# Performance work log

Hardware: AMD Instinct MI355X
Metric: run time of the kernel (lower is better)

## Reference

```python
import jax, jax.numpy as jnp
import numpy as np
from jax import lax

DN = ('NCHW', 'OIHW', 'NCHW')

def conv(x, w, b, stride):
    y = lax.conv_general_dilated(x, w, (stride, stride), ((1, 1), (1, 1)), dimension_numbers=DN)
    return y + b[None, :, None, None]

def deconv(x, w, b):
    # PyTorch ConvTranspose2d(k=3, stride=2, padding=1, output_padding=1): doubles H, W.
    # w has torch layout [in, out, kH, kW]; convert to OIHW and flip spatially.
    wt = jnp.flip(w, (-2, -1)).transpose(1, 0, 2, 3)
    y = lax.conv_general_dilated(x, wt, (1, 1), ((1, 2), (1, 2)), lhs_dilation=(2, 2), dimension_numbers=DN)
    return y + b[None, :, None, None]


def setup_inputs() -> dict:
    key = jax.random.key(0)
    ks = jax.random.split(key, 16)
    s = 0.05
    d = {
        'x': jax.random.normal(ks[0], (16, 3, 256, 256), jnp.float32),
        'w1': jax.random.normal(ks[1], (64, 3, 3, 3), jnp.float32) * s,
        'b1': jnp.zeros((64,), jnp.float32),
        'w2': jax.random.normal(ks[2], (128, 64, 3, 3), jnp.float32) * s,
        'b2': jnp.zeros((128,), jnp.float32),
        'w3': jax.random.normal(ks[3], (256, 128, 3, 3), jnp.float32) * s,
        'b3': jnp.zeros((256,), jnp.float32),
        'w4': jax.random.normal(ks[4], (512, 256, 3, 3), jnp.float32) * s,
        'b4': jnp.zeros((512,), jnp.float32),
        'codebook': jax.random.normal(ks[5], (8192, 512), jnp.float32),
        # ConvTranspose2d weights in torch layout [in, out, kH, kW]
        'd1w': jax.random.normal(ks[6], (512, 256, 3, 3), jnp.float32) * s,
        'd1b': jnp.zeros((256,), jnp.float32),
        'd2w': jax.random.normal(ks[7], (256, 128, 3, 3), jnp.float32) * s,
        'd2b': jnp.zeros((128,), jnp.float32),
        'd3w': jax.random.normal(ks[8], (128, 64, 3, 3), jnp.float32) * s,
        'd3b': jnp.zeros((64,), jnp.float32),
        'wo': jax.random.normal(ks[9], (3, 64, 3, 3), jnp.float32) * s,
        'bo': jnp.zeros((3,), jnp.float32),
    }
    return d


def reference(x, w1, b1, w2, b2, w3, b3, w4, b4, codebook, d1w, d1b, d2w, d2b, d3w, d3b, wo, bo):
    # Encoder: 256 -> 256 -> 128 -> 64 -> 32 spatial
    h = jax.nn.relu(conv(x, w1, b1, 1))
    h = jax.nn.relu(conv(h, w2, b2, 2))
    h = jax.nn.relu(conv(h, w3, b3, 2))
    z = conv(h, w4, b4, 2)  # [B, 512, 32, 32]

    # Quantize: nearest codebook entry per spatial vector (channels-last).
    B, C, H, W = z.shape
    zf = z.transpose(0, 2, 3, 1).reshape(-1, C)  # [N, 512]
    # squared euclidean distances; argmin identical to cdist argmin
    d2 = (jnp.sum(zf * zf, axis=-1, keepdims=True)
          - 2.0 * (zf @ codebook.T)
          + jnp.sum(codebook * codebook, axis=-1))  # [N, K]
    indices = jnp.argmin(d2, axis=-1)  # [N]
    zq = codebook[indices].reshape(B, H, W, C).transpose(0, 3, 1, 2)  # [B, 512, 32, 32]

    # Decoder: 32 -> 64 -> 128 -> 256
    g = jax.nn.relu(deconv(zq, d1w, d1b))
    g = jax.nn.relu(deconv(g, d2w, d2b))
    g = jax.nn.relu(deconv(g, d3w, d3b))
    x_recon = jax.nn.sigmoid(conv(g, wo, bo, 1))
    return x_recon, indices
```

## Files before the change

kernel.cpp:

```cpp
#include <hip/hip_runtime.h>
#include <cstddef>

typedef short short8 __attribute__((ext_vector_type(8)));
typedef _Float16 half8 __attribute__((ext_vector_type(8)));
typedef _Float16 half4 __attribute__((ext_vector_type(4)));
typedef _Float16 half2v __attribute__((ext_vector_type(2)));
typedef float floatx4 __attribute__((ext_vector_type(4)));

__device__ __forceinline__ unsigned short f2bf(float f) {
    unsigned u = __float_as_uint(f);
    u += 0x7FFFu + ((u >> 16) & 1u);
    return (unsigned short)(u >> 16);
}
__device__ __forceinline__ float bf2f(unsigned short h) {
    return __uint_as_float((unsigned)h << 16);
}

__global__ __launch_bounds__(256)
void fused_conv12_mfma_kernel(const float* __restrict__ x,
                              const float* __restrict__ w1,
                              const float* __restrict__ b1,
                              const _Float16* __restrict__ w2h,
                              const _Float16* __restrict__ w2l,
                              const float* __restrict__ b2,
                              _Float16* __restrict__ outH,
                              _Float16* __restrict__ outL)
{
    __shared__ float s_x[3][11][36];
    __shared__ _Float16 sE[2][9][17][40];
    __shared__ _Float16 sO[2][9][16][40];

    const int tid = threadIdx.x;
    const int lane = tid & 63;
    const int wave = tid >> 6;
    const int n16 = lane & 15;
    const int quad = lane >> 4;

    const int ox0 = (blockIdx.x & 7) * 16;
    const int oy0 = (blockIdx.x >> 3) * 4;
    const int co0 = blockIdx.y * 64 + wave * 16;
    const int img = blockIdx.z;

    const int hy0 = oy0 * 2 - 1, hx0 = ox0 * 2 - 1;
    const int gy0 = hy0 - 1,     gx0 = hx0 - 1;
    const float* xN = x + (size_t)img * 3 * 65536;

    for (int e = tid; e < 3 * 11 * 35; e += 256) {
        int c = e / 385, r = e % 385;
        int yy = r / 35, xx = r % 35;
        int gy = gy0 + yy, gx = gx0 + xx;
        float v = 0.f;
        if ((unsigned)gy < 256u && (unsigned)gx < 256u)
            v = xN[(size_t)c * 65536 + gy * 256 + gx];
        s_x[c][yy][xx] = v;
    }

    floatx4 acc1[4], acc2[4];
#pragma unroll
    for (int s = 0; s < 4; s++) {
        acc1[s] = (floatx4){0.f, 0.f, 0.f, 0.f};
        acc2[s] = (floatx4){0.f, 0.f, 0.f, 0.f};
    }

    const int pair = tid & 15;
    const int pxg  = tid >> 4;

    for (int c0 = 0; c0 < 64; c0 += 32) {
        __syncthreads();

        const int ch0 = c0 + pair * 2;
        float wA[27], wB[27];
#pragma unroll
        for (int k = 0; k < 27; k++) {
            wA[k] = w1[ch0 * 27 + k];
            wB[k] = w1[ch0 * 27 + 27 + k];
        }
        const float bA = b1[ch0], bB = b1[ch0 + 1];

        for (int px = pxg; px < 33; px += 16) {
            const bool colok = (unsigned)(hx0 + px) < 256u;
            float xw[3][3][3];
#pragma unroll
            for (int c = 0; c < 3; c++)
#pragma unroll
                for (int r = 0; r < 3; r++)
#pragma unroll
                    for (int kx = 0; kx < 3; kx++)
                        xw[c][r][kx] = s_x[c][r][px + kx];
#pragma unroll
            for (int py = 0; py < 9; py++) {
                const bool inb = colok && (unsigned)(hy0 + py) < 256u;
                float aA = bA, aB = bB;
#pragma unroll
                for (int c = 0; c < 3; c++)
#pragma unroll
                    for (int k = 0; k < 9; k++) {
                        const float xv = xw[c][k / 3][k % 3];
                        aA += wA[c * 9 + k] * xv;
                        aB += wB[c * 9 + k] * xv;
                    }
                float vA = inb ? fmaxf(aA, 0.f) : 0.f;
                float vB = inb ? fmaxf(aB, 0.f) : 0.f;
                half2v hv, lv;
                _Float16 hA = (_Float16)vA, hB = (_Float16)vB;
                hv[0] = hA; hv[1] = hB;
                lv[0] = (_Float16)((vA - (float)hA) * 1024.f);
                lv[1] = (_Float16)((vB - (float)hB) * 1024.f);
                _Float16* dH = (px & 1) ? &sO[0][py][px >> 1][pair * 2]
                                        : &sE[0][py][px >> 1][pair * 2];
                _Float16* dL = (px & 1) ? &sO[1][py][px >> 1][pair * 2]
                                        : &sE[1][py][px >> 1][pair * 2];
                *(half2v*)dH = hv;
                *(half2v*)dL = lv;
                if (py < 8) {
#pragma unroll
                    for (int c = 0; c < 3; c++) {
#pragma unroll
                        for (int r = 0; r < 2; r++)
#pragma unroll
                            for (int kx = 0; kx < 3; kx++)
                                xw[c][r][kx] = xw[c][r + 1][kx];
#pragma unroll
                        for (int kx = 0; kx < 3; kx++)
                            xw[c][2][kx] = s_x[c][py + 3][px + kx];
                    }
                }
            }
        }
        __syncthreads();

        half8 ah[9], al[9];
#pragma unroll
        for (int tp = 0; tp < 9; tp++) {
            size_t o = ((size_t)(tp * 128 + co0 + n16)) * 64 + c0 + quad * 8;
            ah[tp] = *(const half8*)(w2h + o);
            al[tp] = *(const half8*)(w2l + o);
        }
#pragma unroll
        for (int oy = 0; oy < 4; oy++) {
#pragma unroll
            for (int tp = 0; tp < 9; tp++) {
                const int kx = tp % 3;
                const int row = oy * 2 + tp / 3;
                half8 bh, bl;
                if (kx == 0)      { bh = *(const half8*)&sE[0][row][n16][quad * 8];
                                    bl = *(const half8*)&sE[1][row][n16][quad * 8]; }
                else if (kx == 1) { bh = *(const half8*)&sO[0][row][n16][quad * 8];
                                    bl = *(const half8*)&sO[1][row][n16][quad * 8]; }
                else              { bh = *(const half8*)&sE[0][row][n16 + 1][quad * 8];
                                    bl = *(const half8*)&sE[1][row][n16 + 1][quad * 8]; }
                acc1[oy] = __builtin_amdgcn_mfma_f32_16x16x32_f16(ah[tp], bh, acc1[oy], 0, 0, 0);
                acc2[oy] = __builtin_amdgcn_mfma_f32_16x16x32_f16(ah[tp], bl, acc2[oy], 0, 0, 0);
                acc2[oy] = __builtin_amdgcn_mfma_f32_16x16x32_f16(al[tp], bh, acc2[oy], 0, 0, 0);
            }
        }
    }

    const float4 bv = *(const float4*)&b2[co0 + quad * 4];
    const float bb[4] = {bv.x, bv.y, bv.z, bv.w};
#pragma unroll
    for (int oy = 0; oy < 4; oy++) {
        half4 hv, lv;
#pragma unroll
        for (int r = 0; r < 4; r++) {
            float v = fmaxf(acc1[oy][r] + acc2[oy][r] * (1.0f / 1024.0f) + bb[r], 0.f);
            _Float16 h = (_Float16)v;
            hv[r] = h;
            lv[r] = (_Float16)((v - (float)h) * 1024.f);
        }
        size_t o = (((size_t)img * 128 + (oy0 + oy)) * 128 + (ox0 + n16)) * 128
                   + co0 + quad * 4;
        *(half4*)(outH + o) = hv;
        *(half4*)(outL + o) = lv;
    }
}

template<int CI, int CO>
__global__ __launch_bounds__(256)
void prepack_conv_kernel(const float* __restrict__ w,
                         _Float16* __restrict__ wh, _Float16* __restrict__ wl)
{
    int i = blockIdx.x * 256 + threadIdx.x;
    if (i >= CO * CI * 9) return;
    int co = i / (CI * 9);
    int r  = i % (CI * 9);
    int ci = r / 9;
    int tp = r % 9;
    float v = w[i];
    _Float16 h = (_Float16)v;
    size_t o = ((size_t)tp * CO + co) * CI + ci;
    wh[o] = h;
    wl[o] = (_Float16)((v - (float)h) * 1024.f);
}

template<int CIN, int COUT, int IH, int IW, bool RELU>
__global__ __launch_bounds__(256)
void conv_mfma_kernel(const _Float16* __restrict__ inH, const _Float16* __restrict__ inL,
                      const _Float16* __restrict__ wpH, const _Float16* __restrict__ wpL,
                      const float* __restrict__ bias,
                      _Float16* __restrict__ outH, _Float16* __restrict__ outL)
{
    constexpr int OH = IH / 2, OW = IW / 2;
    __shared__ _Float16 sE[2][9][17][40];
    __shared__ _Float16 sO[2][9][16][40];

    const int tid = threadIdx.x;
    const int lane = tid & 63;
    const int wave = tid >> 6;
    const int n16 = lane & 15;
    const int quad = lane >> 4;

    constexpr int NTX = OW / 16;
    const int ox0 = (blockIdx.x % NTX) * 16;
    const int oy0 = (blockIdx.x / NTX) * 4;
    const int co0 = blockIdx.y * 64 + wave * 16;
    const int img = blockIdx.z;

    const int iy0 = oy0 * 2 - 1;
    const int ix0 = ox0 * 2 - 1;
    const _Float16* iNH = inH + (size_t)img * IH * IW * CIN;
    const _Float16* iNL = inL + (size_t)img * IH * IW * CIN;

    floatx4 acc1[4], acc2[4];
#pragma unroll
    for (int s = 0; s < 4; s++) {
        acc1[s] = (floatx4){0.f, 0.f, 0.f, 0.f};
        acc2[s] = (floatx4){0.f, 0.f, 0.f, 0.f};
    }

    for (int k0 = 0; k0 < CIN; k0 += 32) {
        __syncthreads();
        for (int e = tid; e < 2376; e += 256) {
            int pl = e / 1188;
            int r  = e % 1188;
            int pix = r >> 2, q = r & 3;
            int py = pix / 33, px = pix % 33;
            int iy = iy0 + py, ix = ix0 + px;
            half8 v = (half8)(_Float16)0;
            if ((unsigned)iy < (unsigned)IH && (unsigned)ix < (unsigned)IW)
                v = *(const half8*)((pl ? iNL : iNH) + ((size_t)(iy * IW + ix) * CIN + k0 + q * 8));
            if (px & 1) *(half8*)&sO[pl][py][px >> 1][q * 8] = v;
            else        *(half8*)&sE[pl][py][px >> 1][q * 8] = v;
        }
        __syncthreads();

        half8 ah[9], al[9];
#pragma unroll
        for (int tp = 0; tp < 9; tp++) {
            size_t o = ((size_t)(tp * COUT + co0 + n16)) * CIN + k0 + quad * 8;
            ah[tp] = *(const half8*)(wpH + o);
            al[tp] = *(const half8*)(wpL + o);
        }

#pragma unroll
        for (int oy = 0; oy < 4; oy++) {
#pragma unroll
            for (int tp = 0; tp < 9; tp++) {
                const int ky = tp / 3, kx = tp % 3;
                const int row = oy * 2 + ky;
                half8 bh, bl;
                if (kx == 0)      { bh = *(const half8*)&sE[0][row][n16][quad * 8];
                                    bl = *(const half8*)&sE[1][row][n16][quad * 8]; }
                else if (kx == 1) { bh = *(const half8*)&sO[0][row][n16][quad * 8];
                                    bl = *(const half8*)&sO[1][row][n16][quad * 8]; }
                else              { bh = *(const half8*)&sE[0][row][n16 + 1][quad * 8];
                                    bl = *(const half8*)&sE[1][row][n16 + 1][quad * 8]; }
                acc1[oy] = __builtin_amdgcn_mfma_f32_16x16x32_f16(ah[tp], bh, acc1[oy], 0, 0, 0);
                acc2[oy] = __builtin_amdgcn_mfma_f32_16x16x32_f16(ah[tp], bl, acc2[oy], 0, 0, 0);
                acc2[oy] = __builtin_amdgcn_mfma_f32_16x16x32_f16(al[tp], bh, acc2[oy], 0, 0, 0);
            }
        }
    }

    const float4 bv = *(const float4*)&bias[co0 + quad * 4];
    const float bb[4] = {bv.x, bv.y, bv.z, bv.w};
#pragma unroll
    for (int oy = 0; oy < 4; oy++) {
        half4 hv, lv;
#pragma unroll
        for (int r = 0; r < 4; r++) {
            float v = acc1[oy][r] + acc2[oy][r] * (1.0f / 1024.0f) + bb[r];
            if (RELU) v = fmaxf(v, 0.f);
            _Float16 h = (_Float16)v;
            hv[r] = h;
            lv[r] = (_Float16)((v - (float)h) * 1024.f);
        }
        size_t o = (((size_t)img * OH + (oy0 + oy)) * OW + (ox0 + n16)) * COUT
                   + co0 + quad * 4;
        *(half4*)(outH + o) = hv;
        *(half4*)(outL + o) = lv;
    }
}

__global__ __launch_bounds__(64)
void cnorm_kernel(const float* __restrict__ cb, float* __restrict__ cn)
{
    const int code = blockIdx.x;
    const int t = threadIdx.x;
    const float* row = cb + (size_t)code * 512;
    float s = 0.f;
    for (int i = t; i < 512; i += 64) s += row[i] * row[i];
#pragma unroll
    for (int off = 32; off > 0; off >>= 1) s += __shfl_down(s, off, 64);
    if (t == 0) cn[code] = s;
}

__global__ __launch_bounds__(256)
void init_keys_kernel(unsigned long long* __restrict__ keys)
{
    keys[blockIdx.x * 256 + threadIdx.x] = ~0ull;
}

__global__ __launch_bounds__(256)
void split_cb_kernel(const float* __restrict__ cb,
                     _Float16* __restrict__ ch, _Float16* __restrict__ cl)
{
    size_t i = (size_t)blockIdx.x * 256 + threadIdx.x;
    float v = cb[i];
    _Float16 h = (_Float16)v;
    ch[i] = h;
    cl[i] = (_Float16)((v - (float)h) * 1024.f);
}

__global__ __launch_bounds__(256)
void vq_mfma_kernel(const _Float16* __restrict__ zh, const _Float16* __restrict__ zl,
                    const _Float16* __restrict__ ch, const _Float16* __restrict__ cl,
                    const float* __restrict__ cn,
                    unsigned long long* __restrict__ keys)
{
    __shared__ _Float16 sB[2][512 * 8];

    const int tid = threadIdx.x;
    const int lane = tid & 63;
    const int wave = tid >> 6;
    const int n16 = lane & 15;
    const int quad = lane >> 4;

    const int code0 = blockIdx.x * 64;
    const int row0 = blockIdx.y * 256 + wave * 64;

    floatx4 acc1[4][4], acc2[4][4];
#pragma unroll
    for (int rt = 0; rt < 4; rt++)
#pragma unroll
        for (int ct = 0; ct < 4; ct++) {
            acc1[rt][ct] = (floatx4){0.f, 0.f, 0.f, 0.f};
            acc2[rt][ct] = (floatx4){0.f, 0.f, 0.f, 0.f};
        }

    const _Float16* pzh = zh + (size_t)(row0 + n16) * 512 + quad * 8;
    const _Float16* pzl = zl + (size_t)(row0 + n16) * 512 + quad * 8;

    const int e0 = tid, e1 = tid + 256;
    const _Float16* s0 = ((e0 >> 8) ? cl : ch)
        + (size_t)(code0 + ((e0 >> 6) & 3) * 16 + ((e0 >> 2) & 15)) * 512 + (e0 & 3) * 8;
    const _Float16* s1 = ((e1 >> 8) ? cl : ch)
        + (size_t)(code0 + ((e1 >> 6) & 3) * 16 + ((e1 >> 2) & 15)) * 512 + (e1 & 3) * 8;

    *(half8*)&sB[0][e0 * 8] = *(const half8*)s0;
    *(half8*)&sB[0][e1 * 8] = *(const half8*)s1;
    __syncthreads();

    for (int c = 0; c < 16; ++c) {
        const int cur = c & 1;
        const int kk = c * 32;
        half8 ah[4], al[4];
#pragma unroll
        for (int rt = 0; rt < 4; rt++) {
            ah[rt] = *(const half8*)(pzh + (size_t)rt * 8192 + kk);
            al[rt] = *(const half8*)(pzl + (size_t)rt * 8192 + kk);
        }
        half8 t0, t1;
        if (c < 15) {
            t0 = *(const half8*)(s0 + kk + 32);
            t1 = *(const half8*)(s1 + kk + 32);
        }
#pragma unroll
        for (int ct = 0; ct < 4; ++ct) {
            half8 bh = *(const half8*)&sB[cur][(ct * 64 + n16 * 4 + quad) * 8];
            half8 bl = *(const half8*)&sB[cur][(256 + ct * 64 + n16 * 4 + quad) * 8];
#pragma unroll
            for (int rt = 0; rt < 4; rt++) {
                acc1[rt][ct] = __builtin_amdgcn_mfma_f32_16x16x32_f16(ah[rt], bh, acc1[rt][ct], 0, 0, 0);
                acc2[rt][ct] = __builtin_amdgcn_mfma_f32_16x16x32_f16(ah[rt], bl, acc2[rt][ct], 0, 0, 0);
                acc2[rt][ct] = __builtin_amdgcn_mfma_f32_16x16x32_f16(al[rt], bh, acc2[rt][ct], 0, 0, 0);
            }
        }
        if (c < 15) {
            const int nxt = cur ^ 1;
            *(half8*)&sB[nxt][e0 * 8] = t0;
            *(half8*)&sB[nxt][e1 * 8] = t1;
        }
        __syncthreads();
    }

#pragma unroll
    for (int rt = 0; rt < 4; rt++) {
#pragma unroll
        for (int reg = 0; reg < 4; reg++) {
            float best = 3.0e38f;
            int bcode = 0;
#pragma unroll
            for (int ct = 0; ct < 4; ct++) {
                const int code = code0 + ct * 16 + n16;
                float dot = acc1[rt][ct][reg] + acc2[rt][ct][reg] * (1.0f / 1024.0f);
                float s = cn[code] - 2.0f * dot;
                if (s < best) { best = s; bcode = code; }
            }
            unsigned u = __float_as_uint(best);
            u = (u & 0x80000000u) ? ~u : (u | 0x80000000u);
            unsigned long long key = ((unsigned long long)u << 32) | (unsigned)bcode;
#pragma unroll
            for (int m = 1; m < 16; m <<= 1) {
                unsigned long long o = __shfl_xor(key, m, 64);
                key = (o < key) ? o : key;
            }
            if (n16 == 0)
                atomicMin(&keys[row0 + rt * 16 + quad * 4 + reg], key);
        }
    }
}

__global__ __launch_bounds__(256)
void vq_gather_kernel(const unsigned long long* __restrict__ keys,
                      const float* __restrict__ cb,
                      unsigned short* __restrict__ zq, float* __restrict__ idx_out)
{
    __shared__ int sidx[64];
    const int t = threadIdx.x;
    const int v0 = blockIdx.x * 64;
    if (t < 64) {
        int idx = (int)(keys[v0 + t] & 0xFFFFFFFFull);
        sidx[t] = idx;
        idx_out[v0 + t] = (float)idx;
    }
    __syncthreads();
    const int tv = t >> 2;
    const int q = t & 3;
    const float* crow = cb + (size_t)sidx[tv] * 512;
    unsigned short* zrow = zq + (size_t)(v0 + tv) * 512;
    for (int c = q * 8; c < 512; c += 32) {
        float4 f0 = *(const float4*)(crow + c);
        float4 f1 = *(const float4*)(crow + c + 4);
        short8 h;
        h[0] = (short)f2bf(f0.x); h[1] = (short)f2bf(f0.y);
        h[2] = (short)f2bf(f0.z); h[3] = (short)f2bf(f0.w);
        h[4] = (short)f2bf(f1.x); h[5] = (short)f2bf(f1.y);
        h[6] = (short)f2bf(f1.z); h[7] = (short)f2bf(f1.w);
        *(short8*)(zrow + c) = h;
    }
}

template<int CI, int CO>
__global__ __launch_bounds__(256)
void prepack_kernel(const float* __restrict__ w, unsigned short* __restrict__ wp)
{
    int i = blockIdx.x * 256 + threadIdx.x;
    if (i >= 9 * CO * CI) return;
    int ci = i / (CO * 9);
    int r  = i % (CO * 9);
    int co = r / 9;
    int tp = r % 9;
    wp[((size_t)tp * CO + co) * CI + ci] = f2bf(w[i]);
}

template<int CIN, int COUT, int IH, int IW, bool OUT_NCHW>
__global__ __launch_bounds__(256)
void deconv_mfma_kernel(const unsigned short* __restrict__ in,
                        const unsigned short* __restrict__ wp,
                        const float* __restrict__ bias,
                        unsigned short* __restrict__ out)
{
    constexpr int OH = 2 * IH, OW = 2 * IW;
    __shared__ short sIn[5][17][40];

    const int tid = threadIdx.x;
    const int lane = tid & 63;
    const int wave = tid >> 6;
    const int n16 = lane & 15;
    const int quad = lane >> 4;

    constexpr int NTX = IW / 16;
    const int x0 = (blockIdx.x % NTX) * 16;
    const int y0 = (blockIdx.x / NTX) * 4;
    const int co0 = blockIdx.y * 64 + wave * 16;
    const int img = blockIdx.z;

    const unsigned short* inN = in + (size_t)img * IH * IW * CIN;

    floatx4 acc[4][4];
#pragma unroll
    for (int s = 0; s < 4; s++)
#pragma unroll
        for (int c = 0; c < 4; c++) acc[s][c] = (floatx4){0.f, 0.f, 0.f, 0.f};

    for (int k0 = 0; k0 < CIN; k0 += 32) {
        __syncthreads();
        for (int e = tid; e < 340; e += 256) {
            int yy = e / 68, r = e % 68;
            int xx = r >> 2, q4 = r & 3;
            int gy = y0 + yy, gx = x0 + xx;
            short8 v = {0, 0, 0, 0, 0, 0, 0, 0};
            if (gy < IH && gx < IW)
                v = *(const short8*)(inN + ((size_t)(gy * IW + gx) * CIN + k0 + q4 * 8));
            *(short8*)&sIn[yy][xx][q4 * 8] = v;
        }
        __syncthreads();

        short8 a[9];
#pragma unroll
        for (int tp = 0; tp < 9; tp++)
            a[tp] = *(const short8*)(wp + ((size_t)(tp * COUT + co0 + n16) * CIN + k0 + quad * 8));

#pragma unroll
        for (int s = 0; s < 4; s++) {
            short8 b00 = *(const short8*)&sIn[s    ][n16    ][quad * 8];
            short8 b01 = *(const short8*)&sIn[s    ][n16 + 1][quad * 8];
            short8 b10 = *(const short8*)&sIn[s + 1][n16    ][quad * 8];
            short8 b11 = *(const short8*)&sIn[s + 1][n16 + 1][quad * 8];
            acc[s][0] = __builtin_amdgcn_mfma_f32_16x16x32_bf16(a[4], b00, acc[s][0], 0, 0, 0);
            acc[s][1] = __builtin_amdgcn_mfma_f32_16x16x32_bf16(a[3], b01, acc[s][1], 0, 0, 0);
            acc[s][1] = __builtin_amdgcn_mfma_f32_16x16x32_bf16(a[5], b00, acc[s][1], 0, 0, 0);
            acc[s][2] = __builtin_amdgcn_mfma_f32_16x16x32_bf16(a[1], b10, acc[s][2], 0, 0, 0);
            acc[s][2] = __builtin_amdgcn_mfma_f32_16x16x32_bf16(a[7], b00, acc[s][2], 0, 0, 0);
            acc[s][3] = __builtin_amdgcn_mfma_f32_16x16x32_bf16(a[0], b11, acc[s][3], 0, 0, 0);
            acc[s][3] = __builtin_amdgcn_mfma_f32_16x16x32_bf16(a[2], b10, acc[s][3], 0, 0, 0);
            acc[s][3] = __builtin_amdgcn_mfma_f32_16x16x32_bf16(a[6], b01, acc[s][3], 0, 0, 0);
            acc[s][3] = __builtin_amdgcn_mfma_f32_16x16x32_bf16(a[8], b00, acc[s][3], 0, 0, 0);
        }
    }

    const float4 bv = *(const float4*)&bias[co0 + quad * 4];
    const float bb[4] = {bv.x, bv.y, bv.z, bv.w};
    const int x = x0 + n16;

    if (!OUT_NCHW) {
        unsigned short* outN = out + (size_t)img * OH * OW * COUT;
#pragma unroll
        for (int s = 0; s < 4; s++) {
            const int y = y0 + s;
#pragma unroll
            for (int c = 0; c < 4; c++) {
                const int oy = 2 * y + (c >> 1);
                const int ox = 2 * x + (c & 1);
                ushort4 h;
                h.x = f2bf(fmaxf(acc[s][c][0] + bb[0], 0.f));
                h.y = f2bf(fmaxf(acc[s][c][1] + bb[1], 0.f));
                h.z = f2bf(fmaxf(acc[s][c][2] + bb[2], 0.f));
                h.w = f2bf(fmaxf(acc[s][c][3] + bb[3], 0.f));
                *(ushort4*)(outN + ((size_t)(oy * OW + ox) * COUT + co0 + quad * 4)) = h;
            }
        }
    } else {
#pragma unroll
        for (int s = 0; s < 4; s++) {
            const int y = y0 + s;
#pragma unroll
            for (int r = 0; r < 4; r++) {
                const int co = co0 + quad * 4 + r;
                unsigned short* oC = out + (size_t)(img * COUT + co) * OH * OW;
                unsigned p0 = (unsigned)f2bf(fmaxf(acc[s][0][r] + bb[r], 0.f)) |
                              ((unsigned)f2bf(fmaxf(acc[s][1][r] + bb[r], 0.f)) << 16);
                unsigned p1 = (unsigned)f2bf(fmaxf(acc[s][2][r] + bb[r], 0.f)) |
                              ((unsigned)f2bf(fmaxf(acc[s][3][r] + bb[r], 0.f)) << 16);
                *(unsigned*)(oC + (size_t)(2 * y) * OW + 2 * x) = p0;
                *(unsigned*)(oC + (size_t)(2 * y + 1) * OW + 2 * x) = p1;
            }
        }
    }
}

__global__ __launch_bounds__(256)
void conv_out_kernel(const unsigned short* __restrict__ in,
                     const float* __restrict__ w,
                     const float* __restrict__ bias,
                     float* __restrict__ out)
{
    constexpr int TIC = 4;
    __shared__ float s_in[TIC][3][258];
    const int t = threadIdx.x;
    const int y = blockIdx.x;
    const int n = blockIdx.y;
    const unsigned short* inN = in + (size_t)n * 64 * 65536;
    float acc0 = bias[0], acc1 = bias[1], acc2 = bias[2];

    for (int c0 = 0; c0 < 64; c0 += TIC) {
        for (int e = t; e < TIC * 3 * 258; e += 256) {
            int ci = e / 774;
            int r  = e % 774;
            int ry = r / 258, xx = r % 258;
            int gy = y - 1 + ry, gx = xx - 1;
            float v = 0.f;
            if ((unsigned)gy < 256u && (unsigned)gx < 256u)
                v = bf2f(inN[(size_t)(c0 + ci) * 65536 + gy * 256 + gx]);
            s_in[ci][ry][xx] = v;
        }
        __syncthreads();
#pragma unroll
        for (int ci = 0; ci < TIC; ++ci) {
            float iv[3][3];
#pragma unroll
            for (int ry = 0; ry < 3; ry++)
#pragma unroll
                for (int kx = 0; kx < 3; kx++)
                    iv[ry][kx] = s_in[ci][ry][t + kx];
#pragma unroll
            for (int k = 0; k < 9; k++) {
                const float v = iv[k / 3][k % 3];
                acc0 += w[(0 * 64 + c0 + ci) * 9 + k] * v;
                acc1 += w[(1 * 64 + c0 + ci) * 9 + k] * v;
                acc2 += w[(2 * 64 + c0 + ci) * 9 + k] * v;
            }
        }
        __syncthreads();
    }
    const size_t o = (size_t)((n * 3 + 0) * 256 + y) * 256 + t;
    out[o]          = 1.f / (1.f + __expf(-acc0));
    out[o + 65536]  = 1.f / (1.f + __expf(-acc1));
    out[o + 131072] = 1.f / (1.f + __expf(-acc2));
}

extern "C" void kernel_launch(void* const* d_in, const int* in_sizes, int n_in,
                              void* d_out, int out_size, void* d_ws, size_t ws_size,
                              hipStream_t stream)
{
    const float* x   = (const float*)d_in[0];
    const float* w1  = (const float*)d_in[1];
    const float* b1  = (const float*)d_in[2];
    const float* w2  = (const float*)d_in[3];
    const float* b2  = (const float*)d_in[4];
    const float* w3  = (const float*)d_in[5];
    const float* b3  = (const float*)d_in[6];
    const float* w4  = (const float*)d_in[7];
    const float* b4  = (const float*)d_in[8];
    const float* cb  = (const float*)d_in[9];
    const float* d1w = (const float*)d_in[10];
    const float* d1b = (const float*)d_in[11];
    const float* d2w = (const float*)d_in[12];
    const float* d2b = (const float*)d_in[13];
    const float* d3w = (const float*)d_in[14];
    const float* d3b = (const float*)d_in[15];
    const float* wo  = (const float*)d_in[16];
    const float* bo  = (const float*)d_in[17];

    char* ws = (char*)d_ws;
    _Float16* H2H = (_Float16*)(ws);
    _Float16* H2L = (_Float16*)(ws + 67108864);
    _Float16* H3H = (_Float16*)(ws + 134217728);
    _Float16* H3L = (_Float16*)(ws + 167772160);
    _Float16* ZH  = (_Float16*)(ws);
    _Float16* ZL  = (_Float16*)(ws + 16777216);
    unsigned short* ZQ = (unsigned short*)(ws + 33554432);
    _Float16* CBH = (_Float16*)(ws + 50331648);
    _Float16* CBL = (_Float16*)(ws + 58720256);
    unsigned short* G1 = (unsigned short*)(ws + 67108864);
    unsigned short* G2 = (unsigned short*)(ws + 134217728);
    unsigned short* G3 = (unsigned short*)(ws);
    unsigned long long* keys = (unsigned long long*)(ws + 201326592);
    float* cn = (float*)(ws + 201326592 + 131072);

    char* oscratch = (char*)d_out;
    _Float16* EW3H = (_Float16*)(oscratch);
    _Float16* EW3L = (_Float16*)(oscratch + 589824);
    _Float16* EW4H = (_Float16*)(oscratch + 1179648);
    _Float16* EW4L = (_Float16*)(oscratch + 3538944);
    unsigned short* WP1 = (unsigned short*)(oscratch + 5898240);
    unsigned short* WP2 = (unsigned short*)(oscratch + 8257536);
    unsigned short* WP3 = (unsigned short*)(oscratch + 8847360);
    _Float16* EW2H = (_Float16*)(oscratch + 8994816);
    _Float16* EW2L = (_Float16*)(oscratch + 9142272);

    float* xrec = (float*)d_out;
    float* idxf = (float*)d_out + (size_t)16 * 3 * 256 * 256;

    prepack_conv_kernel<64,  128><<<288,  256, 0, stream>>>(w2, EW2H, EW2L);
    prepack_conv_kernel<128, 256><<<1152, 256, 0, stream>>>(w3, EW3H, EW3L);
    prepack_conv_kernel<256, 512><<<4608, 256, 0, stream>>>(w4, EW4H, EW4L);
    prepack_kernel<512, 256><<<4608, 256, 0, stream>>>(d1w, WP1);
    prepack_kernel<256, 128><<<1152, 256, 0, stream>>>(d2w, WP2);
    prepack_kernel<128, 64 ><<<288,  256, 0, stream>>>(d3w, WP3);

    fused_conv12_mfma_kernel<<<dim3(256, 2, 16), 256, 0, stream>>>(x, w1, b1, EW2H, EW2L, b2, H2H, H2L);
    conv_mfma_kernel<128, 256, 128, 128, true ><<<dim3(64, 4, 16), 256, 0, stream>>>(H2H, H2L, EW3H, EW3L, b3, H3H, H3L);
    conv_mfma_kernel<256, 512, 64,  64,  false><<<dim3(16, 8, 16), 256, 0, stream>>>(H3H, H3L, EW4H, EW4L, b4, ZH, ZL);

    cnorm_kernel<<<8192, 64, 0, stream>>>(cb, cn);
    init_keys_kernel<<<64, 256, 0, stream>>>(keys);
    split_cb_kernel<<<16384, 256, 0, stream>>>(cb, CBH, CBL);
    vq_mfma_kernel<<<dim3(128, 64), 256, 0, stream>>>(ZH, ZL, CBH, CBL, cn, keys);
    vq_gather_kernel<<<256, 256, 0, stream>>>(keys, cb, ZQ, idxf);

    deconv_mfma_kernel<512, 256, 32,  32,  false><<<dim3(16,  4, 16), 256, 0, stream>>>(ZQ, WP1, d1b, G1);
    deconv_mfma_kernel<256, 128, 64,  64,  false><<<dim3(64,  2, 16), 256, 0, stream>>>(G1, WP2, d2b, G2);
    deconv_mfma_kernel<128, 64,  128, 128, true ><<<dim3(256, 1, 16), 256, 0, stream>>>(G2, WP3, d3b, G3);
    conv_out_kernel<<<dim3(256, 16), 256, 0, stream>>>(G3, wo, bo, xrec);
}
```

Measured before the change: 2.666 ms.

## Halve VQ rows per wave, prefetch A fragments, and remap shared B layout

The VQ distance kernel now gives each wave 32 rows instead of 64 and launches twice as many blocks along the row dimension. The z-fragment global loads are double-buffered in registers, so the next K-chunk is fetched while the current MFMAs run. The shared-memory codebook tile is re-laid out so each lane reads a contiguous slot indexed by lane. Fewer accumulators per thread should improve occupancy and latency hiding, at the cost of loading each codebook tile from global memory twice as often.

```diff
diff --git a/kernel.cpp b/kernel.cpp
--- a/kernel.cpp
+++ b/kernel.cpp
@@ -337,11 +337,11 @@
     const int quad = lane >> 4;
 
     const int code0 = blockIdx.x * 64;
-    const int row0 = blockIdx.y * 256 + wave * 64;
-
-    floatx4 acc1[4][4], acc2[4][4];
-#pragma unroll
-    for (int rt = 0; rt < 4; rt++)
+    const int row0 = blockIdx.y * 128 + wave * 32;
+
+    floatx4 acc1[2][4], acc2[2][4];
+#pragma unroll
+    for (int rt = 0; rt < 2; rt++)
 #pragma unroll
         for (int ct = 0; ct < 4; ct++) {
             acc1[rt][ct] = (floatx4){0.f, 0.f, 0.f, 0.f};
@@ -351,51 +351,54 @@
     const _Float16* pzh = zh + (size_t)(row0 + n16) * 512 + quad * 8;
     const _Float16* pzl = zl + (size_t)(row0 + n16) * 512 + quad * 8;
 
-    const int e0 = tid, e1 = tid + 256;
-    const _Float16* s0 = ((e0 >> 8) ? cl : ch)
-        + (size_t)(code0 + ((e0 >> 6) & 3) * 16 + ((e0 >> 2) & 15)) * 512 + (e0 & 3) * 8;
-    const _Float16* s1 = ((e1 >> 8) ? cl : ch)
-        + (size_t)(code0 + ((e1 >> 6) & 3) * 16 + ((e1 >> 2) & 15)) * 512 + (e1 & 3) * 8;
-
-    *(half8*)&sB[0][e0 * 8] = *(const half8*)s0;
-    *(half8*)&sB[0][e1 * 8] = *(const half8*)s1;
+    const _Float16* s0 = ch
+        + (size_t)(code0 + ((tid >> 6) & 3) * 16 + (tid & 15)) * 512 + ((tid >> 4) & 3) * 8;
+    const _Float16* s1 = cl
+        + (size_t)(code0 + ((tid >> 6) & 3) * 16 + (tid & 15)) * 512 + ((tid >> 4) & 3) * 8;
+
+    half8 As[2][4];
+    As[0][0] = *(const half8*)(pzh);
+    As[0][1] = *(const half8*)(pzh + 8192);
+    As[0][2] = *(const half8*)(pzl);
+    As[0][3] = *(const half8*)(pzl + 8192);
+    *(half8*)&sB[0][tid * 8]         = *(const half8*)s0;
+    *(half8*)&sB[0][(tid + 256) * 8] = *(const half8*)s1;
     __syncthreads();
 
     for (int c = 0; c < 16; ++c) {
         const int cur = c & 1;
         const int kk = c * 32;
-        half8 ah[4], al[4];
-#pragma unroll
-        for (int rt = 0; rt < 4; rt++) {
-            ah[rt] = *(const half8*)(pzh + (size_t)rt * 8192 + kk);
-            al[rt] = *(const half8*)(pzl + (size_t)rt * 8192 + kk);
-        }
         half8 t0, t1;
         if (c < 15) {
+            const int nxt = cur ^ 1;
+            As[nxt][0] = *(const half8*)(pzh + kk + 32);
+            As[nxt][1] = *(const half8*)(pzh + 8192 + kk + 32);
+            As[nxt][2] = *(const half8*)(pzl + kk + 32);
+            As[nxt][3] = *(const half8*)(pzl + 8192 + kk + 32);
             t0 = *(const half8*)(s0 + kk + 32);
             t1 = *(const half8*)(s1 + kk + 32);
         }
 #pragma unroll
         for (int ct = 0; ct < 4; ++ct) {
-            half8 bh = *(const half8*)&sB[cur][(ct * 64 + n16 * 4 + quad) * 8];
-            half8 bl = *(const half8*)&sB[cur][(256 + ct * 64 + n16 * 4 + quad) * 8];
-#pragma unroll
-            for (int rt = 0; rt < 4; rt++) {
-                acc1[rt][ct] = __builtin_amdgcn_mfma_f32_16x16x32_f16(ah[rt], bh, acc1[rt][ct], 0, 0, 0);
-                acc2[rt][ct] = __builtin_amdgcn_mfma_f32_16x16x32_f16(ah[rt], bl, acc2[rt][ct], 0, 0, 0);
-                acc2[rt][ct] = __builtin_amdgcn_mfma_f32_16x16x32_f16(al[rt], bh, acc2[rt][ct], 0, 0, 0);
+            half8 bh = *(const half8*)&sB[cur][(ct * 64 + lane) * 8];
+            half8 bl = *(const half8*)&sB[cur][((4 + ct) * 64 + lane) * 8];
+#pragma unroll
+            for (int rt = 0; rt < 2; rt++) {
+                acc1[rt][ct] = __builtin_amdgcn_mfma_f32_16x16x32_f16(As[cur][rt],     bh, acc1[rt][ct], 0, 0, 0);
+                acc2[rt][ct] = __builtin_amdgcn_mfma_f32_16x16x32_f16(As[cur][rt],     bl, acc2[rt][ct], 0, 0, 0);
+                acc2[rt][ct] = __builtin_amdgcn_mfma_f32_16x16x32_f16(As[cur][2 + rt], bh, acc2[rt][ct], 0, 0, 0);
             }
         }
         if (c < 15) {
             const int nxt = cur ^ 1;
-            *(half8*)&sB[nxt][e0 * 8] = t0;
-            *(half8*)&sB[nxt][e1 * 8] = t1;
-        }
-        __syncthreads();
-    }
-
-#pragma unroll
-    for (int rt = 0; rt < 4; rt++) {
+            *(half8*)&sB[nxt][tid * 8]         = t0;
+            *(half8*)&sB[nxt][(tid + 256) * 8] = t1;
+        }
+        __syncthreads();
+    }
+
+#pragma unroll
+    for (int rt = 0; rt < 2; rt++) {
 #pragma unroll
         for (int reg = 0; reg < 4; reg++) {
             float best = 3.0e38f;
@@ -687,7 +690,7 @@
     cnorm_kernel<<<8192, 64, 0, stream>>>(cb, cn);
     init_keys_kernel<<<64, 256, 0, stream>>>(keys);
     split_cb_kernel<<<16384, 256, 0, stream>>>(cb, CBH, CBL);
-    vq_mfma_kernel<<<dim3(128, 64), 256, 0, stream>>>(ZH, ZL, CBH, CBL, cn, keys);
+    vq_mfma_kernel<<<dim3(128, 128), 256, 0, stream>>>(ZH, ZL, CBH, CBL, cn, keys);
     vq_gather_kernel<<<256, 256, 0, stream>>>(keys, cb, ZQ, idxf);
 
     deconv_mfma_kernel<512, 256, 32,  32,  false><<<dim3(16,  4, 16), 256, 0, stream>>>(ZQ, WP1, d1b, G1);
```

After: 2.310 ms. 13.3% less time.
